# Kernel tuning notes

Measured on AMD Instinct MI355X. Metric: run time of the kernel, lower is better.

The kernel has to match this reference:

```python
import jax, jax.numpy as jnp
import numpy as np

N_NODES = 100000
N_EDGES = 1600000
EMBED = 64
HEADS = 8
HEAD_DIM = EMBED // HEADS
FFN = 4 * EMBED
EPS = 1e-5


def _layer_norm(x, g, b):
    m = jnp.mean(x, axis=-1, keepdims=True)
    v = jnp.mean(jnp.square(x - m), axis=-1, keepdims=True)
    return (x - m) * jax.lax.rsqrt(v + EPS) * g + b


def setup_inputs() -> dict:
    key = jax.random.key(0)
    ks = jax.random.split(key, 10)
    s = lambda fan_in: 1.0 / np.sqrt(fan_in)
    x = jax.random.normal(ks[0], (N_NODES, EMBED), dtype=jnp.float32)
    edge_indices = jax.random.randint(ks[1], (2, N_EDGES), 0, N_NODES, dtype=jnp.int64)
    attn_w = jax.random.uniform(ks[2], (EMBED, 3 * EMBED), jnp.float32, -s(EMBED), s(EMBED))
    attn_b = jnp.zeros((3 * EMBED,), jnp.float32)
    w1 = jax.random.uniform(ks[3], (EMBED, FFN), jnp.float32, -s(EMBED), s(EMBED))
    b1 = jnp.zeros((FFN,), jnp.float32)
    w2 = jax.random.uniform(ks[4], (FFN, EMBED), jnp.float32, -s(FFN), s(FFN))
    b2 = jnp.zeros((EMBED,), jnp.float32)
    ln1_g = jnp.ones((EMBED,), jnp.float32)
    ln1_b = jnp.zeros((EMBED,), jnp.float32)
    ln2_g = jnp.ones((EMBED,), jnp.float32)
    ln2_b = jnp.zeros((EMBED,), jnp.float32)
    return {"x": x, "edge_indices": edge_indices, "attn_w": attn_w, "attn_b": attn_b,
            "w1": w1, "b1": b1, "w2": w2, "b2": b2,
            "ln1_g": ln1_g, "ln1_b": ln1_b, "ln2_g": ln2_g, "ln2_b": ln2_b}


def _self_attention(x, edge_indices, attn_w, attn_b):
    n = x.shape[0]
    row, col = edge_indices[0], edge_indices[1]
    scale = EMBED ** (-0.5)  # note: original scales by embed_dim**-0.5
    qkv = (x @ attn_w + attn_b).reshape(n, HEADS, 3 * HEAD_DIM)
    q, k, v = jnp.split(qkv, 3, axis=2)  # each [N, H, Dh]
    alpha = jnp.sum(q[row] * k[col], axis=2) * scale  # [E, H]
    # sparse per-row softmax via segment reductions
    m = jax.ops.segment_max(alpha, row, num_segments=n)  # [N, H]
    e = jnp.exp(alpha - m[row])
    denom = jax.ops.segment_sum(e, row, num_segments=n)  # [N, H]
    weights = e / denom[row]  # [E, H]
    vals = v[col] * weights[:, :, None]  # [E, H, Dh]
    out = jax.ops.segment_sum(vals, row, num_segments=n)  # [N, H, Dh]
    return out.reshape(n, EMBED)


def reference(x, edge_indices, attn_w, attn_b, w1, b1, w2, b2, ln1_g, ln1_b, ln2_g, ln2_b):
    # post-norm (norm_first=False), dropout=0
    x = _layer_norm(x + _self_attention(x, edge_indices, attn_w, attn_b), ln1_g, ln1_b)
    ffn = jax.nn.relu(x @ w1 + b1) @ w2 + b2
    x = _layer_norm(x + ffn, ln2_g, ln2_b)
    return x
```

## Files before the change

kernel.cpp:

```cpp
#include <hip/hip_runtime.h>
#include <hip/hip_bf16.h>


#define WAVE 64
constexpr int BUCKET_SHIFT = 7;
constexpr int NBMAX = 800;

typedef __attribute__((ext_vector_type(8))) short bf16x8;
typedef __attribute__((ext_vector_type(4))) float f32x4;
typedef __attribute__((ext_vector_type(2))) float f32x2;
typedef __attribute__((ext_vector_type(2))) _Float16 h16x2;

__device__ __forceinline__ float bfbits_lo(unsigned u) {
  return __uint_as_float(u << 16);
}
__device__ __forceinline__ float bfbits_hi(unsigned u) {
  return __uint_as_float(u & 0xffff0000u);
}
__device__ __forceinline__ unsigned f2bf_pk(float a, float b) {
  unsigned ua = __float_as_uint(a);
  unsigned ub = __float_as_uint(b);
  ua = (ua + 0x7fff + ((ua >> 16) & 1)) >> 16;
  ub = (ub + 0x7fff + ((ub >> 16) & 1)) & 0xffff0000u;
  return ua | ub;
}
__device__ __forceinline__ unsigned short f2bf1(float a) {
  unsigned ua = __float_as_uint(a);
  ua = (ua + 0x7fff + ((ua >> 16) & 1)) >> 16;
  return (unsigned short)ua;
}

#if defined(__has_builtin)
#if __has_builtin(__builtin_amdgcn_cvt_pkrtz)
#define HAS_PKRTZ 1
#endif
#if __has_builtin(__builtin_amdgcn_fdot2)
#define HAS_FDOT2 1
#endif
#endif
#define EXP2F(x) exp2f(x)

__device__ __forceinline__ unsigned f2h_pk(float a, float b) {
#ifdef HAS_PKRTZ
  auto h = __builtin_amdgcn_cvt_pkrtz(a, b);
  return __builtin_bit_cast(unsigned, h);
#else
  h16x2 h;
  h.x = (_Float16)a;
  h.y = (_Float16)b;
  return __builtin_bit_cast(unsigned, h);
#endif
}

__device__ __forceinline__ float dot8_f16(uint4 kw, uint4 qw) {
#ifdef HAS_FDOT2
  float s = __builtin_amdgcn_fdot2(__builtin_bit_cast(h16x2, kw.x),
                                   __builtin_bit_cast(h16x2, qw.x), 0.f, false);
  s = __builtin_amdgcn_fdot2(__builtin_bit_cast(h16x2, kw.y),
                             __builtin_bit_cast(h16x2, qw.y), s, false);
  s = __builtin_amdgcn_fdot2(__builtin_bit_cast(h16x2, kw.z),
                             __builtin_bit_cast(h16x2, qw.z), s, false);
  s = __builtin_amdgcn_fdot2(__builtin_bit_cast(h16x2, kw.w),
                             __builtin_bit_cast(h16x2, qw.w), s, false);
  return s;
#else
  unsigned kk[4] = {kw.x, kw.y, kw.z, kw.w};
  unsigned qq[4] = {qw.x, qw.y, qw.z, qw.w};
  float s = 0.f;
#pragma unroll
  for (int i = 0; i < 4; i++) {
    h16x2 a = __builtin_bit_cast(h16x2, kk[i]);
    h16x2 b = __builtin_bit_cast(h16x2, qq[i]);
    s += (float)a.x * (float)b.x + (float)a.y * (float)b.y;
  }
  return s;
#endif
}

__device__ __forceinline__ void accmix8(uint4 w, float e, float acc[8]) {
  h16x2 p;
  p = __builtin_bit_cast(h16x2, w.x);
  acc[0] += (float)p.x * e;
  acc[1] += (float)p.y * e;
  p = __builtin_bit_cast(h16x2, w.y);
  acc[2] += (float)p.x * e;
  acc[3] += (float)p.y * e;
  p = __builtin_bit_cast(h16x2, w.z);
  acc[4] += (float)p.x * e;
  acc[5] += (float)p.y * e;
  p = __builtin_bit_cast(h16x2, w.w);
  acc[6] += (float)p.x * e;
  acc[7] += (float)p.y * e;
}

__global__ __launch_bounds__(256) void cvt_w2(
    const float* __restrict__ aw, const float* __restrict__ w1,
    const float* __restrict__ w2, unsigned short* __restrict__ awT,
    unsigned short* __restrict__ w1T, unsigned short* __restrict__ w2T) {
  int tid = blockIdx.x * 256 + threadIdx.x;
  int stride = gridDim.x * 256;
  for (int i = tid; i < 192 * 64; i += stride) {
    int nn = i >> 6, kk = i & 63;
    awT[i] = f2bf1(aw[kk * 192 + nn]);
  }
  for (int i = tid; i < 256 * 64; i += stride) {
    int nn = i >> 6, kk = i & 63;
    w1T[i] = f2bf1(w1[kk * 256 + nn]);
  }
  for (int i = tid; i < 64 * 256; i += stride) {
    int nn = i >> 8, kk = i & 255;
    w2T[i] = f2bf1(w2[kk * 64 + nn]);
  }
}

template <int NCOLS, int K, int MODE>
__global__ __launch_bounds__(256) void mfma_gemm(
    const unsigned short* __restrict__ A, const float* __restrict__ Af,
    const unsigned short* __restrict__ BT, const float* __restrict__ bias,
    unsigned short* __restrict__ out_q, unsigned char* __restrict__ out_kv,
    unsigned short* __restrict__ out_h,
    const unsigned short* __restrict__ resid, const float* __restrict__ g,
    const float* __restrict__ beta, float* __restrict__ out_f, int n) {
  constexpr int KP = K + 8;
  constexpr int NT = NCOLS / 16;
  constexpr int NKC = K / 32;
  __shared__ unsigned short sB[NCOLS * KP];

  const int tid = threadIdx.x;
  {
    const uint4* src = (const uint4*)BT;
    for (int idx = tid; idx < NCOLS * K / 8; idx += 256) {
      int nn = idx / (K / 8), kq = idx % (K / 8);
      *(uint4*)&sB[nn * KP + kq * 8] = src[idx];
    }
  }
  __syncthreads();

  const int wid = tid >> 6, lane = tid & 63;
  const int l15 = lane & 15, quad = lane >> 4;
  const int rowbase = blockIdx.x * 128 + wid * 32;

  bf16x8 afrag[2][NKC];
#pragma unroll
  for (int rg = 0; rg < 2; rg++) {
    int row = rowbase + rg * 16 + l15;
    if (row >= n) row = n - 1;
    if constexpr (MODE == 0) {
      const float4* ap = (const float4*)(Af + (size_t)row * K);
#pragma unroll
      for (int kc = 0; kc < NKC; kc++) {
        float4 a = ap[kc * 8 + quad * 2], b = ap[kc * 8 + quad * 2 + 1];
        union {
          unsigned u[4];
          bf16x8 v;
        } z;
        z.u[0] = f2bf_pk(a.x, a.y);
        z.u[1] = f2bf_pk(a.z, a.w);
        z.u[2] = f2bf_pk(b.x, b.y);
        z.u[3] = f2bf_pk(b.z, b.w);
        afrag[rg][kc] = z.v;
      }
    } else {
      const bf16x8* ap = (const bf16x8*)(A + (size_t)row * K);
#pragma unroll
      for (int kc = 0; kc < NKC; kc++) afrag[rg][kc] = ap[kc * 4 + quad];
    }
  }

  f32x4 acc[2][NT];
#pragma unroll
  for (int rg = 0; rg < 2; rg++)
#pragma unroll
    for (int t = 0; t < NT; t++) acc[rg][t] = (f32x4){0.f, 0.f, 0.f, 0.f};

#pragma unroll
  for (int t = 0; t < NT; t++) {
#pragma unroll
    for (int kc = 0; kc < NKC; kc++) {
      bf16x8 b = *(const bf16x8*)&sB[(t * 16 + l15) * KP + kc * 32 + quad * 8];
      acc[0][t] = __builtin_amdgcn_mfma_f32_16x16x32_bf16(b, afrag[0][kc],
                                                          acc[0][t], 0, 0, 0);
      acc[1][t] = __builtin_amdgcn_mfma_f32_16x16x32_bf16(b, afrag[1][kc],
                                                          acc[1][t], 0, 0, 0);
    }
  }

  if (MODE == 0) {
    constexpr float QSCALE = 0.125f * 1.44269504088896f;
#pragma unroll
    for (int rg = 0; rg < 2; rg++) {
      int row = rowbase + rg * 16 + l15;
      if (row >= n) continue;
#pragma unroll
      for (int t = 0; t < NT; t++) {
        int c0 = t * 16 + quad * 4;
        float4 bb = *(const float4*)&bias[c0];
        float v0 = acc[rg][t].x + bb.x, v1 = acc[rg][t].y + bb.y;
        float v2 = acc[rg][t].z + bb.z, v3 = acc[rg][t].w + bb.w;
        int hh = c0 / 24, rem = c0 % 24;
        if (rem < 8) {
          v0 *= QSCALE;
          v1 *= QSCALE;
          v2 *= QSCALE;
          v3 *= QSCALE;
          *(uint2*)(out_q + (size_t)row * 64 + hh * 8 + rem) =
              make_uint2(f2h_pk(v0, v1), f2h_pk(v2, v3));
        } else if (rem < 16) {
          *(uint2*)(out_kv + ((size_t)row << 8) + hh * 16 + (rem - 8) * 2) =
              make_uint2(f2h_pk(v0, v1), f2h_pk(v2, v3));
        } else {
          *(uint2*)(out_kv + ((size_t)row << 8) + 128 + hh * 16 +
                    (rem - 16) * 2) =
              make_uint2(f2h_pk(v0, v1), f2h_pk(v2, v3));
        }
      }
    }
  } else if (MODE == 1) {
#pragma unroll
    for (int rg = 0; rg < 2; rg++) {
      int row = rowbase + rg * 16 + l15;
      if (row >= n) continue;
#pragma unroll
      for (int t = 0; t < NT; t++) {
        int c0 = t * 16 + quad * 4;
        float4 bb = *(const float4*)&bias[c0];
        float v0 = fmaxf(acc[rg][t].x + bb.x, 0.f);
        float v1 = fmaxf(acc[rg][t].y + bb.y, 0.f);
        float v2 = fmaxf(acc[rg][t].z + bb.z, 0.f);
        float v3 = fmaxf(acc[rg][t].w + bb.w, 0.f);
        *(uint2*)(out_h + (size_t)row * NCOLS + c0) =
            make_uint2(f2bf_pk(v0, v1), f2bf_pk(v2, v3));
      }
    }
  } else {
#pragma unroll
    for (int rg = 0; rg < 2; rg++) {
      int row = rowbase + rg * 16 + l15;
      bool ok = row < n;
      int rowc = ok ? row : n - 1;
      float vals[4][4];
      float ps = 0.f, pq = 0.f;
#pragma unroll
      for (int t = 0; t < 4; t++) {
        int c0 = t * 16 + quad * 4;
        float4 bb = *(const float4*)&bias[c0];
        uint2 rr = *(const uint2*)&resid[(size_t)rowc * 64 + c0];
        vals[t][0] = acc[rg][t].x + bb.x + bfbits_lo(rr.x);
        vals[t][1] = acc[rg][t].y + bb.y + bfbits_hi(rr.x);
        vals[t][2] = acc[rg][t].z + bb.z + bfbits_lo(rr.y);
        vals[t][3] = acc[rg][t].w + bb.w + bfbits_hi(rr.y);
#pragma unroll
        for (int r = 0; r < 4; r++) {
          ps += vals[t][r];
          pq += vals[t][r] * vals[t][r];
        }
      }
      ps += __shfl_xor(ps, 16);
      ps += __shfl_xor(ps, 32);
      pq += __shfl_xor(pq, 16);
      pq += __shfl_xor(pq, 32);
      float mean = ps * (1.f / 64.f);
      float var = pq * (1.f / 64.f) - mean * mean;
      float inv = rsqrtf(var + 1e-5f);
      if (ok) {
#pragma unroll
        for (int t = 0; t < 4; t++) {
          int c0 = t * 16 + quad * 4;
          float4 gg = *(const float4*)&g[c0];
          float4 be = *(const float4*)&beta[c0];
          float4 o = make_float4((vals[t][0] - mean) * inv * gg.x + be.x,
                                 (vals[t][1] - mean) * inv * gg.y + be.y,
                                 (vals[t][2] - mean) * inv * gg.z + be.z,
                                 (vals[t][3] - mean) * inv * gg.w + be.w);
          *(float4*)&out_f[(size_t)row * 64 + c0] = o;
        }
      }
    }
  }
}

__device__ __forceinline__ int edge_row(const int* e, int i, bool is64) {
  return is64 ? e[2 * (size_t)i] : e[i];
}
__device__ __forceinline__ int edge_col(const int* e, int i, int E, bool is64) {
  return is64 ? e[2 * ((size_t)E + i)] : e[(size_t)E + i];
}

__global__ __launch_bounds__(256) void partition_count(
    const int* __restrict__ e, int E, int* __restrict__ G, int NB, int CH) {
  __shared__ int h[NBMAX];
  __shared__ int s32;
  if (threadIdx.x == 0) s32 = 0;
  for (int b = threadIdx.x; b < NB; b += 256) h[b] = 0;
  __syncthreads();
  unsigned v = 0;
  for (int i = threadIdx.x; i < 2048; i += 256) v |= (unsigned)e[2 * i + 1];
  if (v) s32 = 1;
  __syncthreads();
  bool is64 = (s32 == 0);
  int c0 = blockIdx.x * CH, c1 = min(E, c0 + CH);
  for (int i = c0 + threadIdx.x; i < c1; i += 256)
    atomicAdd(&h[edge_row(e, i, is64) >> BUCKET_SHIFT], 1);
  __syncthreads();
  for (int b = threadIdx.x; b < NB; b += 256) G[b * 256 + blockIdx.x] = h[b];
}

__global__ __launch_bounds__(1024) void scan_reduce(const int* __restrict__ in,
                                                    int n,
                                                    int* __restrict__ bsum) {
  __shared__ int sdata[16];
  int tid = threadIdx.x;
  int idx = blockIdx.x * 1024 + tid;
  int v = (idx < n) ? in[idx] : 0;
#pragma unroll
  for (int m = 1; m < WAVE; m <<= 1) v += __shfl_xor(v, m);
  if ((tid & 63) == 0) sdata[tid >> 6] = v;
  __syncthreads();
  if (tid < 16) {
    int s = sdata[tid];
#pragma unroll
    for (int m = 1; m < 16; m <<= 1) s += __shfl_xor(s, m);
    if (tid == 0) bsum[blockIdx.x] = s;
  }
}

__global__ __launch_bounds__(256) void scan_top(const int* __restrict__ bsum,
                                                int nb,
                                                int* __restrict__ bpre) {
  __shared__ int wsum[4];
  int tid = threadIdx.x;
  int lane = tid & 63, wid = tid >> 6;
  int v = (tid < nb) ? bsum[tid] : 0;
  int incl = v;
#pragma unroll
  for (int m = 1; m < WAVE; m <<= 1) {
    int t = __shfl_up(incl, m);
    if (lane >= m) incl += t;
  }
  if (lane == 63) wsum[wid] = incl;
  __syncthreads();
  int add = 0;
  for (int w = 0; w < wid; w++) add += wsum[w];
  if (tid < nb) bpre[tid] = add + incl - v;
}

__global__ __launch_bounds__(1024) void scan_apply(
    const int* __restrict__ in, int n, const int* __restrict__ bpre,
    int* __restrict__ outscan) {
  __shared__ int wtot[16];
  __shared__ int wexcl[16];
  int tid = threadIdx.x;
  int idx = blockIdx.x * 1024 + tid;
  int v = (idx < n) ? in[idx] : 0;
  int incl = v;
#pragma unroll
  for (int m = 1; m < WAVE; m <<= 1) {
    int t = __shfl_up(incl, m);
    if ((tid & 63) >= m) incl += t;
  }
  int wid = tid >> 6;
  if ((tid & 63) == 63) wtot[wid] = incl;
  __syncthreads();
  if (tid < 16) {
    int w = wtot[tid];
    int wi = w;
#pragma unroll
    for (int m = 1; m < 16; m <<= 1) {
      int t = __shfl_up(wi, m);
      if (tid >= m) wi += t;
    }
    wexcl[tid] = wi - w;
  }
  __syncthreads();
  if (idx < n) outscan[idx] = bpre[blockIdx.x] + wexcl[wid] + incl - v;
}

__global__ __launch_bounds__(256) void partition_scatter(
    const int* __restrict__ e, int E, const int* __restrict__ scanG,
    unsigned* __restrict__ ebuf, int NB, int CH) {
  __shared__ int base[NBMAX];
  __shared__ int s32;
  if (threadIdx.x == 0) s32 = 0;
  for (int b = threadIdx.x; b < NB; b += 256)
    base[b] = scanG[b * 256 + blockIdx.x];
  __syncthreads();
  unsigned v = 0;
  for (int i = threadIdx.x; i < 2048; i += 256) v |= (unsigned)e[2 * i + 1];
  if (v) s32 = 1;
  __syncthreads();
  bool is64 = (s32 == 0);
  int c0 = blockIdx.x * CH, c1 = min(E, c0 + CH);
  for (int i = c0 + threadIdx.x; i < c1; i += 256) {
    int r = edge_row(e, i, is64);
    int c = edge_col(e, i, E, is64);
    int pos = atomicAdd(&base[r >> BUCKET_SHIFT], 1);
    ebuf[pos] = ((unsigned)(r & 127) << 17) | (unsigned)c;
  }
}

__global__ __launch_bounds__(256) void bucket_csr(
    const unsigned* __restrict__ ebuf, const int* __restrict__ scanG,
    int* __restrict__ ecol, int* __restrict__ rowstart, int n, int NB, int E) {
  __shared__ int cnt[128], offs[128], cur[128];
  const int b = blockIdx.x;
  const int tid = threadIdx.x;
  const int start = scanG[b * 256];
  const int end = (b + 1 < NB) ? scanG[(b + 1) * 256] : E;
  if (tid < 128) cnt[tid] = 0;
  __syncthreads();
  for (int i = start + tid; i < end; i += 256)
    atomicAdd(&cnt[(ebuf[i] >> 17) & 127], 1);
  __syncthreads();
  if (tid < 128) offs[tid] = cnt[tid];
  __syncthreads();
  for (int s = 1; s < 128; s <<= 1) {
    int t = 0;
    if (tid < 128 && tid >= s) t = offs[tid - s];
    __syncthreads();
    if (tid < 128) offs[tid] += t;
    __syncthreads();
  }
  if (tid < 128) {
    int excl = offs[tid] - cnt[tid];
    cur[tid] = start + excl;
    int gr = (b << BUCKET_SHIFT) + tid;
    if (gr < n) rowstart[gr] = start + excl;
  }
  if (b == NB - 1 && tid == 0) rowstart[n] = E;
  __syncthreads();
  for (int i = start + tid; i < end; i += 256) {
    unsigned p = ebuf[i];
    int pos = atomicAdd(&cur[(p >> 17) & 127], 1);
    ecol[pos] = (int)(p & 0x1FFFF);
  }
}

__global__ __launch_bounds__(256) void attn_ln_kernel(
    const float* __restrict__ x, const unsigned short* __restrict__ qbuf,
    const unsigned char* __restrict__ kv, const int* __restrict__ rowstart,
    const int* __restrict__ ecol, const float* __restrict__ g,
    const float* __restrict__ beta, unsigned short* __restrict__ x1b, int n) {
  int wave = threadIdx.x >> 6;
  int lane = threadIdx.x & 63;
  int node0 = (blockIdx.x * 4 + wave) * 2;
  if (node0 >= n) return;
  const int e = lane >> 4;
  const int h = lane & 7;
  int node = node0 + ((lane >> 3) & 1);
  bool nvalid = node < n;
  int nodec = nvalid ? node : n - 1;

  uint4 qp = ((const uint4*)qbuf)[(size_t)nodec * 8 + h];

  const float* xr = x + (size_t)nodec * 64 + h * 8;
  float4 x0 = *(const float4*)xr;
  float4 x1 = *(const float4*)(xr + 4);

  int start = rowstart[nodec];
  int cnt = nvalid ? rowstart[nodec + 1] - start : 0;
  const int* ec = ecol + start;
  const int koff = h * 16, voff = 128 + h * 16;

  float den = 0.f;
  float acc[8] = {0.f, 0.f, 0.f, 0.f, 0.f, 0.f, 0.f, 0.f};

  int iters = (cnt + 3) >> 2;
  int maxit = max(iters, __shfl_xor(iters, 8));

  int it = 0;
  for (; it + 2 <= maxit; it += 2) {
    int i0 = it * 4 + e;
    int i1 = i0 + 4;
    bool b0 = i0 < cnt;
    bool b1 = i1 < cnt;
    int c0 = ec[b0 ? i0 : 0] & 0x1FFFF;
    int c1 = ec[b1 ? i1 : 0] & 0x1FFFF;
    const unsigned char* r0 = kv + ((size_t)c0 << 8);
    const unsigned char* r1 = kv + ((size_t)c1 << 8);
    uint4 kw0 = *(const uint4*)(r0 + koff);
    uint4 vw0 = *(const uint4*)(r0 + voff);
    uint4 kw1 = *(const uint4*)(r1 + koff);
    uint4 vw1 = *(const uint4*)(r1 + voff);
    float a0 = dot8_f16(kw0, qp);
    float a1 = dot8_f16(kw1, qp);
    float e0 = b0 ? EXP2F(a0) : 0.f;
    float e1 = b1 ? EXP2F(a1) : 0.f;
    den += e0 + e1;
    accmix8(vw0, e0, acc);
    accmix8(vw1, e1, acc);
  }
  if (it < maxit) {
    int i0 = it * 4 + e;
    bool b0 = i0 < cnt;
    int c0 = ec[b0 ? i0 : 0] & 0x1FFFF;
    const unsigned char* r0 = kv + ((size_t)c0 << 8);
    uint4 kw0 = *(const uint4*)(r0 + koff);
    uint4 vw0 = *(const uint4*)(r0 + voff);
    float a0 = dot8_f16(kw0, qp);
    float e0 = b0 ? EXP2F(a0) : 0.f;
    den += e0;
    accmix8(vw0, e0, acc);
  }

#pragma unroll
  for (int m = 16; m < 64; m <<= 1) {
    den += __shfl_xor(den, m);
#pragma unroll
    for (int j = 0; j < 8; j++) acc[j] += __shfl_xor(acc[j], m);
  }

  float invden = (cnt > 0) ? 1.f / den : 0.f;

  float v[8];
  v[0] = x0.x + acc[0] * invden;
  v[1] = x0.y + acc[1] * invden;
  v[2] = x0.z + acc[2] * invden;
  v[3] = x0.w + acc[3] * invden;
  v[4] = x1.x + acc[4] * invden;
  v[5] = x1.y + acc[5] * invden;
  v[6] = x1.z + acc[6] * invden;
  v[7] = x1.w + acc[7] * invden;

  float ps = 0.f;
#pragma unroll
  for (int j = 0; j < 8; j++) ps += v[j];
#pragma unroll
  for (int m = 1; m < 8; m <<= 1) ps += __shfl_xor(ps, m);
  float mean = ps * (1.f / 64.f);
  float pq = 0.f;
#pragma unroll
  for (int j = 0; j < 8; j++) {
    float d = v[j] - mean;
    pq += d * d;
  }
#pragma unroll
  for (int m = 1; m < 8; m <<= 1) pq += __shfl_xor(pq, m);
  float inv = rsqrtf(pq * (1.f / 64.f) + 1e-5f);

  if (e == 0 && nvalid) {
    const float4* gr = (const float4*)(g + h * 8);
    const float4* br = (const float4*)(beta + h * 8);
    float4 ga = gr[0], gb = gr[1];
    float4 ba = br[0], bb = br[1];
    float o[8];
    o[0] = (v[0] - mean) * inv * ga.x + ba.x;
    o[1] = (v[1] - mean) * inv * ga.y + ba.y;
    o[2] = (v[2] - mean) * inv * ga.z + ba.z;
    o[3] = (v[3] - mean) * inv * ga.w + ba.w;
    o[4] = (v[4] - mean) * inv * gb.x + bb.x;
    o[5] = (v[5] - mean) * inv * gb.y + bb.y;
    o[6] = (v[6] - mean) * inv * gb.z + bb.z;
    o[7] = (v[7] - mean) * inv * gb.w + bb.w;
    *(uint4*)(x1b + (size_t)node * 64 + h * 8) =
        make_uint4(f2bf_pk(o[0], o[1]), f2bf_pk(o[2], o[3]),
                   f2bf_pk(o[4], o[5]), f2bf_pk(o[6], o[7]));
  }
}

extern "C" void kernel_launch(void* const* d_in, const int* in_sizes, int n_in,
                              void* d_out, int out_size, void* d_ws,
                              size_t ws_size, hipStream_t stream) {
  const float* x = (const float*)d_in[0];
  const int* edges = (const int*)d_in[1];
  const float* attn_w = (const float*)d_in[2];
  const float* attn_b = (const float*)d_in[3];
  const float* w1 = (const float*)d_in[4];
  const float* b1 = (const float*)d_in[5];
  const float* w2 = (const float*)d_in[6];
  const float* b2 = (const float*)d_in[7];
  const float* g1 = (const float*)d_in[8];
  const float* bb1 = (const float*)d_in[9];
  const float* g2 = (const float*)d_in[10];
  const float* bb2 = (const float*)d_in[11];

  const int N = in_sizes[0] / 64;
  const int E = in_sizes[1] / 2;
  const int NB = (N + 127) >> BUCKET_SHIFT;
  const int CH = (E + 255) / 256;
  const int NG = NB * 256;

  char* ws = (char*)d_ws;
  size_t oq = 0;
  size_t okv = oq + (size_t)N * 128;
  size_t ox1b = okv + (size_t)N * 256;
  size_t oh = ox1b + (size_t)N * 128;
  size_t oawT = oh + (size_t)N * 512;
  size_t ow1T = oawT + 192 * 64 * 2;
  size_t ow2T = ow1T + 256 * 64 * 2;
  size_t oG = ow2T + 64 * 256 * 2;
  size_t oscanG = oG + (size_t)NG * 4;
  size_t oebuf = oscanG + (size_t)NG * 4;
  size_t oecol = oebuf + (size_t)E * 4;
  size_t orowstart = oecol + (size_t)E * 4;
  size_t obsum = orowstart + (size_t)(N + 4) * 4;
  size_t obpre = obsum + 1024;

  unsigned short* qbuf = (unsigned short*)(ws + oq);
  unsigned char* kvb = (unsigned char*)(ws + okv);
  unsigned short* x1b = (unsigned short*)(ws + ox1b);
  unsigned short* hbuf = (unsigned short*)(ws + oh);
  unsigned short* awT = (unsigned short*)(ws + oawT);
  unsigned short* w1T = (unsigned short*)(ws + ow1T);
  unsigned short* w2T = (unsigned short*)(ws + ow2T);
  int* G = (int*)(ws + oG);
  int* scanG = (int*)(ws + oscanG);
  unsigned* ebuf = (unsigned*)(ws + oebuf);
  int* ecol = (int*)(ws + oecol);
  int* rowstart = (int*)(ws + orowstart);
  int* bsum = (int*)(ws + obsum);
  int* bpre = (int*)(ws + obpre);

  cvt_w2<<<32, 256, 0, stream>>>(attn_w, w1, w2, awT, w1T, w2T);

  partition_count<<<256, 256, 0, stream>>>(edges, E, G, NB, CH);
  int nscan = (NG + 1023) / 1024;
  scan_reduce<<<nscan, 1024, 0, stream>>>(G, NG, bsum);
  scan_top<<<1, 256, 0, stream>>>(bsum, nscan, bpre);
  scan_apply<<<nscan, 1024, 0, stream>>>(G, NG, bpre, scanG);
  partition_scatter<<<256, 256, 0, stream>>>(edges, E, scanG, ebuf, NB, CH);
  bucket_csr<<<NB, 256, 0, stream>>>(ebuf, scanG, ecol, rowstart, N, NB, E);

  const int gblocks = (N + 127) / 128;

  mfma_gemm<192, 64, 0><<<gblocks, 256, 0, stream>>>(
      nullptr, x, awT, attn_b, qbuf, kvb, nullptr, nullptr, nullptr, nullptr,
      nullptr, N);

  attn_ln_kernel<<<(N + 7) / 8, 256, 0, stream>>>(x, qbuf, kvb, rowstart, ecol,
                                                  g1, bb1, x1b, N);

  mfma_gemm<256, 64, 1><<<gblocks, 256, 0, stream>>>(
      x1b, nullptr, w1T, b1, nullptr, nullptr, hbuf, nullptr, nullptr, nullptr,
      nullptr, N);

  mfma_gemm<64, 256, 2><<<gblocks, 256, 0, stream>>>(
      hbuf, nullptr, w2T, b2, nullptr, nullptr, nullptr, x1b, g2, bb2,
      (float*)d_out, N);
}
```

Measured before the change: 289.9 us.

## Increase edge-partition block count and halve GEMM rows per block

Raises the partition_count/partition_scatter grid from 256 to 1024 blocks, with a smaller edge chunk per block. The histogram matrix and the scan grow to match, and scan_top becomes a 1024-thread looping scan that can handle more than 256 partial sums. The MFMA GEMMs now give each wave 16 rows instead of 32, doubling the number of blocks so more of the GPU is busy. The int64 edge reads use an int2 view. In exchange, the scan has four times more histogram entries to process, and each GEMM block loads the shared B tile while reusing it across fewer rows.

```diff
diff --git a/kernel.cpp b/kernel.cpp
--- a/kernel.cpp
+++ b/kernel.cpp
@@ -5,6 +5,7 @@
 #define WAVE 64
 constexpr int BUCKET_SHIFT = 7;
 constexpr int NBMAX = 800;
+constexpr int NBLK = 1024;
 
 typedef __attribute__((ext_vector_type(8))) short bf16x8;
 typedef __attribute__((ext_vector_type(4))) float f32x4;
@@ -138,65 +139,54 @@
 
   const int wid = tid >> 6, lane = tid & 63;
   const int l15 = lane & 15, quad = lane >> 4;
-  const int rowbase = blockIdx.x * 128 + wid * 32;
-
-  bf16x8 afrag[2][NKC];
-#pragma unroll
-  for (int rg = 0; rg < 2; rg++) {
-    int row = rowbase + rg * 16 + l15;
-    if (row >= n) row = n - 1;
-    if constexpr (MODE == 0) {
-      const float4* ap = (const float4*)(Af + (size_t)row * K);
-#pragma unroll
-      for (int kc = 0; kc < NKC; kc++) {
-        float4 a = ap[kc * 8 + quad * 2], b = ap[kc * 8 + quad * 2 + 1];
-        union {
-          unsigned u[4];
-          bf16x8 v;
-        } z;
-        z.u[0] = f2bf_pk(a.x, a.y);
-        z.u[1] = f2bf_pk(a.z, a.w);
-        z.u[2] = f2bf_pk(b.x, b.y);
-        z.u[3] = f2bf_pk(b.z, b.w);
-        afrag[rg][kc] = z.v;
-      }
-    } else {
-      const bf16x8* ap = (const bf16x8*)(A + (size_t)row * K);
-#pragma unroll
-      for (int kc = 0; kc < NKC; kc++) afrag[rg][kc] = ap[kc * 4 + quad];
-    }
-  }
-
-  f32x4 acc[2][NT];
-#pragma unroll
-  for (int rg = 0; rg < 2; rg++)
-#pragma unroll
-    for (int t = 0; t < NT; t++) acc[rg][t] = (f32x4){0.f, 0.f, 0.f, 0.f};
+  const int row0 = blockIdx.x * 64 + wid * 16 + l15;
+  const int row = (row0 < n) ? row0 : (n - 1);
+
+  bf16x8 afrag[NKC];
+  if constexpr (MODE == 0) {
+    const float4* ap = (const float4*)(Af + (size_t)row * K);
+#pragma unroll
+    for (int kc = 0; kc < NKC; kc++) {
+      float4 a = ap[kc * 8 + quad * 2], b = ap[kc * 8 + quad * 2 + 1];
+      union {
+        unsigned u[4];
+        bf16x8 v;
+      } z;
+      z.u[0] = f2bf_pk(a.x, a.y);
+      z.u[1] = f2bf_pk(a.z, a.w);
+      z.u[2] = f2bf_pk(b.x, b.y);
+      z.u[3] = f2bf_pk(b.z, b.w);
+      afrag[kc] = z.v;
+    }
+  } else {
+    const bf16x8* ap = (const bf16x8*)(A + (size_t)row * K);
+#pragma unroll
+    for (int kc = 0; kc < NKC; kc++) afrag[kc] = ap[kc * 4 + quad];
+  }
+
+  f32x4 acc[NT];
+#pragma unroll
+  for (int t = 0; t < NT; t++) acc[t] = (f32x4){0.f, 0.f, 0.f, 0.f};
 
 #pragma unroll
   for (int t = 0; t < NT; t++) {
 #pragma unroll
     for (int kc = 0; kc < NKC; kc++) {
       bf16x8 b = *(const bf16x8*)&sB[(t * 16 + l15) * KP + kc * 32 + quad * 8];
-      acc[0][t] = __builtin_amdgcn_mfma_f32_16x16x32_bf16(b, afrag[0][kc],
-                                                          acc[0][t], 0, 0, 0);
-      acc[1][t] = __builtin_amdgcn_mfma_f32_16x16x32_bf16(b, afrag[1][kc],
-                                                          acc[1][t], 0, 0, 0);
+      acc[t] =
+          __builtin_amdgcn_mfma_f32_16x16x32_bf16(b, afrag[kc], acc[t], 0, 0, 0);
     }
   }
 
   if (MODE == 0) {
     constexpr float QSCALE = 0.125f * 1.44269504088896f;
-#pragma unroll
-    for (int rg = 0; rg < 2; rg++) {
-      int row = rowbase + rg * 16 + l15;
-      if (row >= n) continue;
+    if (row0 < n) {
 #pragma unroll
       for (int t = 0; t < NT; t++) {
         int c0 = t * 16 + quad * 4;
         float4 bb = *(const float4*)&bias[c0];
-        float v0 = acc[rg][t].x + bb.x, v1 = acc[rg][t].y + bb.y;
-        float v2 = acc[rg][t].z + bb.z, v3 = acc[rg][t].w + bb.w;
+        float v0 = acc[t].x + bb.x, v1 = acc[t].y + bb.y;
+        float v2 = acc[t].z + bb.z, v3 = acc[t].w + bb.w;
         int hh = c0 / 24, rem = c0 % 24;
         if (rem < 8) {
           v0 *= QSCALE;
@@ -216,74 +206,66 @@
       }
     }
   } else if (MODE == 1) {
-#pragma unroll
-    for (int rg = 0; rg < 2; rg++) {
-      int row = rowbase + rg * 16 + l15;
-      if (row >= n) continue;
+    if (row0 < n) {
 #pragma unroll
       for (int t = 0; t < NT; t++) {
         int c0 = t * 16 + quad * 4;
         float4 bb = *(const float4*)&bias[c0];
-        float v0 = fmaxf(acc[rg][t].x + bb.x, 0.f);
-        float v1 = fmaxf(acc[rg][t].y + bb.y, 0.f);
-        float v2 = fmaxf(acc[rg][t].z + bb.z, 0.f);
-        float v3 = fmaxf(acc[rg][t].w + bb.w, 0.f);
+        float v0 = fmaxf(acc[t].x + bb.x, 0.f);
+        float v1 = fmaxf(acc[t].y + bb.y, 0.f);
+        float v2 = fmaxf(acc[t].z + bb.z, 0.f);
+        float v3 = fmaxf(acc[t].w + bb.w, 0.f);
         *(uint2*)(out_h + (size_t)row * NCOLS + c0) =
             make_uint2(f2bf_pk(v0, v1), f2bf_pk(v2, v3));
       }
     }
   } else {
-#pragma unroll
-    for (int rg = 0; rg < 2; rg++) {
-      int row = rowbase + rg * 16 + l15;
-      bool ok = row < n;
-      int rowc = ok ? row : n - 1;
-      float vals[4][4];
-      float ps = 0.f, pq = 0.f;
+    bool ok = row0 < n;
+    float vals[4][4];
+    float ps = 0.f, pq = 0.f;
+#pragma unroll
+    for (int t = 0; t < 4; t++) {
+      int c0 = t * 16 + quad * 4;
+      float4 bb = *(const float4*)&bias[c0];
+      uint2 rr = *(const uint2*)&resid[(size_t)row * 64 + c0];
+      vals[t][0] = acc[t].x + bb.x + bfbits_lo(rr.x);
+      vals[t][1] = acc[t].y + bb.y + bfbits_hi(rr.x);
+      vals[t][2] = acc[t].z + bb.z + bfbits_lo(rr.y);
+      vals[t][3] = acc[t].w + bb.w + bfbits_hi(rr.y);
+#pragma unroll
+      for (int r = 0; r < 4; r++) {
+        ps += vals[t][r];
+        pq += vals[t][r] * vals[t][r];
+      }
+    }
+    ps += __shfl_xor(ps, 16);
+    ps += __shfl_xor(ps, 32);
+    pq += __shfl_xor(pq, 16);
+    pq += __shfl_xor(pq, 32);
+    float mean = ps * (1.f / 64.f);
+    float var = pq * (1.f / 64.f) - mean * mean;
+    float inv = rsqrtf(var + 1e-5f);
+    if (ok) {
 #pragma unroll
       for (int t = 0; t < 4; t++) {
         int c0 = t * 16 + quad * 4;
-        float4 bb = *(const float4*)&bias[c0];
-        uint2 rr = *(const uint2*)&resid[(size_t)rowc * 64 + c0];
-        vals[t][0] = acc[rg][t].x + bb.x + bfbits_lo(rr.x);
-        vals[t][1] = acc[rg][t].y + bb.y + bfbits_hi(rr.x);
-        vals[t][2] = acc[rg][t].z + bb.z + bfbits_lo(rr.y);
-        vals[t][3] = acc[rg][t].w + bb.w + bfbits_hi(rr.y);
-#pragma unroll
-        for (int r = 0; r < 4; r++) {
-          ps += vals[t][r];
-          pq += vals[t][r] * vals[t][r];
-        }
+        float4 gg = *(const float4*)&g[c0];
+        float4 be = *(const float4*)&beta[c0];
+        float4 o = make_float4((vals[t][0] - mean) * inv * gg.x + be.x,
+                               (vals[t][1] - mean) * inv * gg.y + be.y,
+                               (vals[t][2] - mean) * inv * gg.z + be.z,
+                               (vals[t][3] - mean) * inv * gg.w + be.w);
+        *(float4*)&out_f[(size_t)row * 64 + c0] = o;
       }
-      ps += __shfl_xor(ps, 16);
-      ps += __shfl_xor(ps, 32);
-      pq += __shfl_xor(pq, 16);
-      pq += __shfl_xor(pq, 32);
-      float mean = ps * (1.f / 64.f);
-      float var = pq * (1.f / 64.f) - mean * mean;
-      float inv = rsqrtf(var + 1e-5f);
-      if (ok) {
-#pragma unroll
-        for (int t = 0; t < 4; t++) {
-          int c0 = t * 16 + quad * 4;
-          float4 gg = *(const float4*)&g[c0];
-          float4 be = *(const float4*)&beta[c0];
-          float4 o = make_float4((vals[t][0] - mean) * inv * gg.x + be.x,
-                                 (vals[t][1] - mean) * inv * gg.y + be.y,
-                                 (vals[t][2] - mean) * inv * gg.z + be.z,
-                                 (vals[t][3] - mean) * inv * gg.w + be.w);
-          *(float4*)&out_f[(size_t)row * 64 + c0] = o;
-        }
-      }
     }
   }
 }
 
 __device__ __forceinline__ int edge_row(const int* e, int i, bool is64) {
-  return is64 ? e[2 * (size_t)i] : e[i];
+  return is64 ? ((const int2*)e)[i].x : e[i];
 }
 __device__ __forceinline__ int edge_col(const int* e, int i, int E, bool is64) {
-  return is64 ? e[2 * ((size_t)E + i)] : e[(size_t)E + i];
+  return is64 ? ((const int2*)e)[(size_t)E + i].x : e[(size_t)E + i];
 }
 
 __global__ __launch_bounds__(256) void partition_count(
@@ -302,7 +284,7 @@
   for (int i = c0 + threadIdx.x; i < c1; i += 256)
     atomicAdd(&h[edge_row(e, i, is64) >> BUCKET_SHIFT], 1);
   __syncthreads();
-  for (int b = threadIdx.x; b < NB; b += 256) G[b * 256 + blockIdx.x] = h[b];
+  for (int b = threadIdx.x; b < NB; b += 256) G[b * NBLK + blockIdx.x] = h[b];
 }
 
 __global__ __launch_bounds__(1024) void scan_reduce(const int* __restrict__ in,
@@ -324,24 +306,36 @@
   }
 }
 
-__global__ __launch_bounds__(256) void scan_top(const int* __restrict__ bsum,
-                                                int nb,
-                                                int* __restrict__ bpre) {
-  __shared__ int wsum[4];
-  int tid = threadIdx.x;
-  int lane = tid & 63, wid = tid >> 6;
-  int v = (tid < nb) ? bsum[tid] : 0;
-  int incl = v;
-#pragma unroll
-  for (int m = 1; m < WAVE; m <<= 1) {
-    int t = __shfl_up(incl, m);
-    if (lane >= m) incl += t;
-  }
-  if (lane == 63) wsum[wid] = incl;
-  __syncthreads();
-  int add = 0;
-  for (int w = 0; w < wid; w++) add += wsum[w];
-  if (tid < nb) bpre[tid] = add + incl - v;
+__global__ __launch_bounds__(1024) void scan_top(const int* __restrict__ bsum,
+                                                 int nb,
+                                                 int* __restrict__ bpre) {
+  __shared__ int wsum[16];
+  __shared__ int carry;
+  int tid = threadIdx.x, lane = tid & 63, wid = tid >> 6;
+  if (tid == 0) carry = 0;
+  __syncthreads();
+  for (int base = 0; base < nb; base += 1024) {
+    int idx = base + tid;
+    int v = (idx < nb) ? bsum[idx] : 0;
+    int incl = v;
+#pragma unroll
+    for (int m = 1; m < WAVE; m <<= 1) {
+      int t = __shfl_up(incl, m);
+      if (lane >= m) incl += t;
+    }
+    if (lane == 63) wsum[wid] = incl;
+    __syncthreads();
+    int add = carry;
+    for (int w = 0; w < wid; w++) add += wsum[w];
+    if (idx < nb) bpre[idx] = add + incl - v;
+    __syncthreads();
+    if (tid == 0) {
+      int t = 0;
+      for (int w = 0; w < 16; w++) t += wsum[w];
+      carry += t;
+    }
+    __syncthreads();
+  }
 }
 
 __global__ __launch_bounds__(1024) void scan_apply(
@@ -382,7 +376,7 @@
   __shared__ int s32;
   if (threadIdx.x == 0) s32 = 0;
   for (int b = threadIdx.x; b < NB; b += 256)
-    base[b] = scanG[b * 256 + blockIdx.x];
+    base[b] = scanG[b * NBLK + blockIdx.x];
   __syncthreads();
   unsigned v = 0;
   for (int i = threadIdx.x; i < 2048; i += 256) v |= (unsigned)e[2 * i + 1];
@@ -404,8 +398,8 @@
   __shared__ int cnt[128], offs[128], cur[128];
   const int b = blockIdx.x;
   const int tid = threadIdx.x;
-  const int start = scanG[b * 256];
-  const int end = (b + 1 < NB) ? scanG[(b + 1) * 256] : E;
+  const int start = scanG[b * NBLK];
+  const int end = (b + 1 < NB) ? scanG[(b + 1) * NBLK] : E;
   if (tid < 128) cnt[tid] = 0;
   __syncthreads();
   for (int i = start + tid; i < end; i += 256)
@@ -576,8 +570,8 @@
   const int N = in_sizes[0] / 64;
   const int E = in_sizes[1] / 2;
   const int NB = (N + 127) >> BUCKET_SHIFT;
-  const int CH = (E + 255) / 256;
-  const int NG = NB * 256;
+  const int CH = (E + NBLK - 1) / NBLK;
+  const int NG = NB * NBLK;
 
   char* ws = (char*)d_ws;
   size_t oq = 0;
@@ -593,7 +587,7 @@
   size_t oecol = oebuf + (size_t)E * 4;
   size_t orowstart = oecol + (size_t)E * 4;
   size_t obsum = orowstart + (size_t)(N + 4) * 4;
-  size_t obpre = obsum + 1024;
+  size_t obpre = obsum + 4096;
 
   unsigned short* qbuf = (unsigned short*)(ws + oq);
   unsigned char* kvb = (unsigned char*)(ws + okv);
@@ -612,15 +606,15 @@
 
   cvt_w2<<<32, 256, 0, stream>>>(attn_w, w1, w2, awT, w1T, w2T);
 
-  partition_count<<<256, 256, 0, stream>>>(edges, E, G, NB, CH);
+  partition_count<<<NBLK, 256, 0, stream>>>(edges, E, G, NB, CH);
   int nscan = (NG + 1023) / 1024;
   scan_reduce<<<nscan, 1024, 0, stream>>>(G, NG, bsum);
-  scan_top<<<1, 256, 0, stream>>>(bsum, nscan, bpre);
+  scan_top<<<1, 1024, 0, stream>>>(bsum, nscan, bpre);
   scan_apply<<<nscan, 1024, 0, stream>>>(G, NG, bpre, scanG);
-  partition_scatter<<<256, 256, 0, stream>>>(edges, E, scanG, ebuf, NB, CH);
+  partition_scatter<<<NBLK, 256, 0, stream>>>(edges, E, scanG, ebuf, NB, CH);
   bucket_csr<<<NB, 256, 0, stream>>>(ebuf, scanG, ecol, rowstart, N, NB, E);
 
-  const int gblocks = (N + 127) / 128;
+  const int gblocks = (N + 63) / 64;
 
   mfma_gemm<192, 64, 0><<<gblocks, 256, 0, stream>>>(
       nullptr, x, awT, attn_b, qbuf, kvb, nullptr, nullptr, nullptr, nullptr,
```

New measurement: 297.5 us. 2.6% more time.

## Collapse edge partition pipeline into fewer kernels and switch GEMMs to fp16

Applied to the files above, without the earlier changes.

Replaces the seven-kernel CSR build (count, three-pass scan, scatter, bucket) with a memset plus three kernels. Global bucket counts are now accumulated with atomics, and each block scans those counts locally, so the separate scan launches go away. The weight conversion is folded into the counting kernel. All bf16 intermediates and MFMAs are switched to fp16, which gives more mantissa bits but a narrower range. The scatter order now depends on atomics, so the edge order inside a bucket is no longer deterministic.

```diff
diff --git a/kernel.cpp b/kernel.cpp
--- a/kernel.cpp
+++ b/kernel.cpp
@@ -1,55 +1,28 @@
 #include <hip/hip_runtime.h>
-#include <hip/hip_bf16.h>
 
 
 #define WAVE 64
 constexpr int BUCKET_SHIFT = 7;
 constexpr int NBMAX = 800;
 
-typedef __attribute__((ext_vector_type(8))) short bf16x8;
+typedef __attribute__((ext_vector_type(8))) short s16x8;
 typedef __attribute__((ext_vector_type(4))) float f32x4;
-typedef __attribute__((ext_vector_type(2))) float f32x2;
 typedef __attribute__((ext_vector_type(2))) _Float16 h16x2;
-
-__device__ __forceinline__ float bfbits_lo(unsigned u) {
-  return __uint_as_float(u << 16);
-}
-__device__ __forceinline__ float bfbits_hi(unsigned u) {
-  return __uint_as_float(u & 0xffff0000u);
-}
-__device__ __forceinline__ unsigned f2bf_pk(float a, float b) {
-  unsigned ua = __float_as_uint(a);
-  unsigned ub = __float_as_uint(b);
-  ua = (ua + 0x7fff + ((ua >> 16) & 1)) >> 16;
-  ub = (ub + 0x7fff + ((ub >> 16) & 1)) & 0xffff0000u;
-  return ua | ub;
-}
-__device__ __forceinline__ unsigned short f2bf1(float a) {
-  unsigned ua = __float_as_uint(a);
-  ua = (ua + 0x7fff + ((ua >> 16) & 1)) >> 16;
-  return (unsigned short)ua;
-}
+typedef __attribute__((ext_vector_type(8))) __fp16 fp16x8;
 
 #if defined(__has_builtin)
-#if __has_builtin(__builtin_amdgcn_cvt_pkrtz)
-#define HAS_PKRTZ 1
-#endif
 #if __has_builtin(__builtin_amdgcn_fdot2)
 #define HAS_FDOT2 1
 #endif
 #endif
 #define EXP2F(x) exp2f(x)
 
+__device__ __forceinline__ unsigned short f2h1(float a) {
+  _Float16 h = (_Float16)a;
+  return __builtin_bit_cast(unsigned short, h);
+}
 __device__ __forceinline__ unsigned f2h_pk(float a, float b) {
-#ifdef HAS_PKRTZ
-  auto h = __builtin_amdgcn_cvt_pkrtz(a, b);
-  return __builtin_bit_cast(unsigned, h);
-#else
-  h16x2 h;
-  h.x = (_Float16)a;
-  h.y = (_Float16)b;
-  return __builtin_bit_cast(unsigned, h);
-#endif
+  return (unsigned)f2h1(a) | ((unsigned)f2h1(b) << 16);
 }
 
 __device__ __forceinline__ float dot8_f16(uint4 kw, uint4 qw) {
@@ -93,23 +66,152 @@
   acc[7] += (float)p.y * e;
 }
 
-__global__ __launch_bounds__(256) void cvt_w2(
+__device__ __forceinline__ int edge_row(const int* e, int i, bool is64) {
+  return is64 ? e[2 * (size_t)i] : e[i];
+}
+__device__ __forceinline__ int edge_col(const int* e, int i, int E, bool is64) {
+  return is64 ? e[2 * ((size_t)E + i)] : e[(size_t)E + i];
+}
+
+__device__ __forceinline__ void scan_buckets(const int* __restrict__ bcnt,
+                                             int NB, int* sb) {
+  __shared__ int ws_[4];
+  int tid = threadIdx.x;
+  int t0 = tid * 4;
+  int v0 = 0, v1 = 0, v2 = 0, v3 = 0;
+  if (t0 + 0 < NB) v0 = bcnt[t0 + 0];
+  if (t0 + 1 < NB) v1 = bcnt[t0 + 1];
+  if (t0 + 2 < NB) v2 = bcnt[t0 + 2];
+  if (t0 + 3 < NB) v3 = bcnt[t0 + 3];
+  int s = v0 + v1 + v2 + v3;
+  int lane = tid & 63, wid = tid >> 6;
+  int incl = s;
+#pragma unroll
+  for (int m = 1; m < WAVE; m <<= 1) {
+    int t = __shfl_up(incl, m);
+    if (lane >= m) incl += t;
+  }
+  if (lane == 63) ws_[wid] = incl;
+  __syncthreads();
+  int add = 0;
+  for (int w = 0; w < wid; w++) add += ws_[w];
+  int base = add + incl - s;
+  if (t0 + 0 < NB) sb[t0 + 0] = base;
+  base += v0;
+  if (t0 + 1 < NB) sb[t0 + 1] = base;
+  base += v1;
+  if (t0 + 2 < NB) sb[t0 + 2] = base;
+  base += v2;
+  if (t0 + 3 < NB) sb[t0 + 3] = base;
+  __syncthreads();
+}
+
+__global__ __launch_bounds__(256) void prep_kernel(
     const float* __restrict__ aw, const float* __restrict__ w1,
     const float* __restrict__ w2, unsigned short* __restrict__ awT,
-    unsigned short* __restrict__ w1T, unsigned short* __restrict__ w2T) {
-  int tid = blockIdx.x * 256 + threadIdx.x;
+    unsigned short* __restrict__ w1T, unsigned short* __restrict__ w2T,
+    const int* __restrict__ e, int E, int* __restrict__ bcnt, int NB, int CH) {
+  int gtid = blockIdx.x * 256 + threadIdx.x;
   int stride = gridDim.x * 256;
-  for (int i = tid; i < 192 * 64; i += stride) {
+  for (int i = gtid; i < 192 * 64; i += stride) {
     int nn = i >> 6, kk = i & 63;
-    awT[i] = f2bf1(aw[kk * 192 + nn]);
-  }
-  for (int i = tid; i < 256 * 64; i += stride) {
+    awT[i] = f2h1(aw[kk * 192 + nn]);
+  }
+  for (int i = gtid; i < 256 * 64; i += stride) {
     int nn = i >> 6, kk = i & 63;
-    w1T[i] = f2bf1(w1[kk * 256 + nn]);
-  }
-  for (int i = tid; i < 64 * 256; i += stride) {
+    w1T[i] = f2h1(w1[kk * 256 + nn]);
+  }
+  for (int i = gtid; i < 64 * 256; i += stride) {
     int nn = i >> 8, kk = i & 255;
-    w2T[i] = f2bf1(w2[kk * 64 + nn]);
+    w2T[i] = f2h1(w2[kk * 64 + nn]);
+  }
+  __shared__ int h[NBMAX];
+  __shared__ int s32;
+  if (threadIdx.x == 0) s32 = 0;
+  for (int b = threadIdx.x; b < NB; b += 256) h[b] = 0;
+  __syncthreads();
+  unsigned v = 0;
+  for (int i = threadIdx.x; i < 2048; i += 256) v |= (unsigned)e[2 * i + 1];
+  if (v) s32 = 1;
+  __syncthreads();
+  bool is64 = (s32 == 0);
+  int c0 = blockIdx.x * CH, c1 = min(E, c0 + CH);
+  for (int i = c0 + threadIdx.x; i < c1; i += 256)
+    atomicAdd(&h[edge_row(e, i, is64) >> BUCKET_SHIFT], 1);
+  __syncthreads();
+  for (int b = threadIdx.x; b < NB; b += 256)
+    if (h[b]) atomicAdd(&bcnt[b], h[b]);
+}
+
+__global__ __launch_bounds__(256) void scatter_kernel(
+    const int* __restrict__ e, int E, const int* __restrict__ bcnt,
+    int* __restrict__ gcur, unsigned* __restrict__ ebuf, int NB, int CH) {
+  __shared__ int h[NBMAX];
+  __shared__ int sb[NBMAX];
+  __shared__ int cur[NBMAX];
+  __shared__ int s32;
+  if (threadIdx.x == 0) s32 = 0;
+  for (int b = threadIdx.x; b < NB; b += 256) h[b] = 0;
+  __syncthreads();
+  unsigned v = 0;
+  for (int i = threadIdx.x; i < 2048; i += 256) v |= (unsigned)e[2 * i + 1];
+  if (v) s32 = 1;
+  __syncthreads();
+  bool is64 = (s32 == 0);
+  int c0 = blockIdx.x * CH, c1 = min(E, c0 + CH);
+  for (int i = c0 + threadIdx.x; i < c1; i += 256)
+    atomicAdd(&h[edge_row(e, i, is64) >> BUCKET_SHIFT], 1);
+  __syncthreads();
+  scan_buckets(bcnt, NB, sb);
+  for (int b = threadIdx.x; b < NB; b += 256) {
+    int hb = h[b];
+    cur[b] = hb ? (sb[b] + atomicAdd(&gcur[b], hb)) : 0;
+  }
+  __syncthreads();
+  for (int i = c0 + threadIdx.x; i < c1; i += 256) {
+    int r = edge_row(e, i, is64);
+    int c = edge_col(e, i, E, is64);
+    int pos = atomicAdd(&cur[r >> BUCKET_SHIFT], 1);
+    ebuf[pos] = ((unsigned)(r & 127) << 17) | (unsigned)c;
+  }
+}
+
+__global__ __launch_bounds__(256) void bucket_csr(
+    const unsigned* __restrict__ ebuf, const int* __restrict__ bcnt,
+    int* __restrict__ ecol, int* __restrict__ rowstart, int n, int NB, int E) {
+  __shared__ int cnt[128], offs[128], cur[128];
+  __shared__ int sb[NBMAX];
+  scan_buckets(bcnt, NB, sb);
+  const int b = blockIdx.x;
+  const int tid = threadIdx.x;
+  const int start = sb[b];
+  const int end = (b + 1 < NB) ? sb[b + 1] : E;
+  if (tid < 128) cnt[tid] = 0;
+  __syncthreads();
+  for (int i = start + tid; i < end; i += 256)
+    atomicAdd(&cnt[(ebuf[i] >> 17) & 127], 1);
+  __syncthreads();
+  if (tid < 128) offs[tid] = cnt[tid];
+  __syncthreads();
+  for (int s = 1; s < 128; s <<= 1) {
+    int t = 0;
+    if (tid < 128 && tid >= s) t = offs[tid - s];
+    __syncthreads();
+    if (tid < 128) offs[tid] += t;
+    __syncthreads();
+  }
+  if (tid < 128) {
+    int excl = offs[tid] - cnt[tid];
+    cur[tid] = start + excl;
+    int gr = (b << BUCKET_SHIFT) + tid;
+    if (gr < n) rowstart[gr] = start + excl;
+  }
+  if (b == NB - 1 && tid == 0) rowstart[n] = E;
+  __syncthreads();
+  for (int i = start + tid; i < end; i += 256) {
+    unsigned p = ebuf[i];
+    int pos = atomicAdd(&cur[(p >> 17) & 127], 1);
+    ecol[pos] = (int)(p & 0x1FFFF);
   }
 }
 
@@ -140,7 +242,7 @@
   const int l15 = lane & 15, quad = lane >> 4;
   const int rowbase = blockIdx.x * 128 + wid * 32;
 
-  bf16x8 afrag[2][NKC];
+  s16x8 afrag[2][NKC];
 #pragma unroll
   for (int rg = 0; rg < 2; rg++) {
     int row = rowbase + rg * 16 + l15;
@@ -152,16 +254,16 @@
         float4 a = ap[kc * 8 + quad * 2], b = ap[kc * 8 + quad * 2 + 1];
         union {
           unsigned u[4];
-          bf16x8 v;
+          s16x8 v;
         } z;
-        z.u[0] = f2bf_pk(a.x, a.y);
-        z.u[1] = f2bf_pk(a.z, a.w);
-        z.u[2] = f2bf_pk(b.x, b.y);
-        z.u[3] = f2bf_pk(b.z, b.w);
+        z.u[0] = f2h_pk(a.x, a.y);
+        z.u[1] = f2h_pk(a.z, a.w);
+        z.u[2] = f2h_pk(b.x, b.y);
+        z.u[3] = f2h_pk(b.z, b.w);
         afrag[rg][kc] = z.v;
       }
     } else {
-      const bf16x8* ap = (const bf16x8*)(A + (size_t)row * K);
+      const s16x8* ap = (const s16x8*)(A + (size_t)row * K);
 #pragma unroll
       for (int kc = 0; kc < NKC; kc++) afrag[rg][kc] = ap[kc * 4 + quad];
     }
@@ -177,11 +279,12 @@
   for (int t = 0; t < NT; t++) {
 #pragma unroll
     for (int kc = 0; kc < NKC; kc++) {
-      bf16x8 b = *(const bf16x8*)&sB[(t * 16 + l15) * KP + kc * 32 + quad * 8];
-      acc[0][t] = __builtin_amdgcn_mfma_f32_16x16x32_bf16(b, afrag[0][kc],
-                                                          acc[0][t], 0, 0, 0);
-      acc[1][t] = __builtin_amdgcn_mfma_f32_16x16x32_bf16(b, afrag[1][kc],
-                                                          acc[1][t], 0, 0, 0);
+      s16x8 b = *(const s16x8*)&sB[(t * 16 + l15) * KP + kc * 32 + quad * 8];
+      fp16x8 bh = __builtin_bit_cast(fp16x8, b);
+      acc[0][t] = __builtin_amdgcn_mfma_f32_16x16x32_f16(
+          bh, __builtin_bit_cast(fp16x8, afrag[0][kc]), acc[0][t], 0, 0, 0);
+      acc[1][t] = __builtin_amdgcn_mfma_f32_16x16x32_f16(
+          bh, __builtin_bit_cast(fp16x8, afrag[1][kc]), acc[1][t], 0, 0, 0);
     }
   }
 
@@ -229,7 +332,7 @@
         float v2 = fmaxf(acc[rg][t].z + bb.z, 0.f);
         float v3 = fmaxf(acc[rg][t].w + bb.w, 0.f);
         *(uint2*)(out_h + (size_t)row * NCOLS + c0) =
-            make_uint2(f2bf_pk(v0, v1), f2bf_pk(v2, v3));
+            make_uint2(f2h_pk(v0, v1), f2h_pk(v2, v3));
       }
     }
   } else {
@@ -245,10 +348,12 @@
         int c0 = t * 16 + quad * 4;
         float4 bb = *(const float4*)&bias[c0];
         uint2 rr = *(const uint2*)&resid[(size_t)rowc * 64 + c0];
-        vals[t][0] = acc[rg][t].x + bb.x + bfbits_lo(rr.x);
-        vals[t][1] = acc[rg][t].y + bb.y + bfbits_hi(rr.x);
-        vals[t][2] = acc[rg][t].z + bb.z + bfbits_lo(rr.y);
-        vals[t][3] = acc[rg][t].w + bb.w + bfbits_hi(rr.y);
+        h16x2 ra = __builtin_bit_cast(h16x2, rr.x);
+        h16x2 rb = __builtin_bit_cast(h16x2, rr.y);
+        vals[t][0] = acc[rg][t].x + bb.x + (float)ra.x;
+        vals[t][1] = acc[rg][t].y + bb.y + (float)ra.y;
+        vals[t][2] = acc[rg][t].z + bb.z + (float)rb.x;
+        vals[t][3] = acc[rg][t].w + bb.w + (float)rb.y;
 #pragma unroll
         for (int r = 0; r < 4; r++) {
           ps += vals[t][r];
@@ -276,162 +381,6 @@
         }
       }
     }
-  }
-}
-
-__device__ __forceinline__ int edge_row(const int* e, int i, bool is64) {
-  return is64 ? e[2 * (size_t)i] : e[i];
-}
-__device__ __forceinline__ int edge_col(const int* e, int i, int E, bool is64) {
-  return is64 ? e[2 * ((size_t)E + i)] : e[(size_t)E + i];
-}
-
-__global__ __launch_bounds__(256) void partition_count(
-    const int* __restrict__ e, int E, int* __restrict__ G, int NB, int CH) {
-  __shared__ int h[NBMAX];
-  __shared__ int s32;
-  if (threadIdx.x == 0) s32 = 0;
-  for (int b = threadIdx.x; b < NB; b += 256) h[b] = 0;
-  __syncthreads();
-  unsigned v = 0;
-  for (int i = threadIdx.x; i < 2048; i += 256) v |= (unsigned)e[2 * i + 1];
-  if (v) s32 = 1;
-  __syncthreads();
-  bool is64 = (s32 == 0);
-  int c0 = blockIdx.x * CH, c1 = min(E, c0 + CH);
-  for (int i = c0 + threadIdx.x; i < c1; i += 256)
-    atomicAdd(&h[edge_row(e, i, is64) >> BUCKET_SHIFT], 1);
-  __syncthreads();
-  for (int b = threadIdx.x; b < NB; b += 256) G[b * 256 + blockIdx.x] = h[b];
-}
-
-__global__ __launch_bounds__(1024) void scan_reduce(const int* __restrict__ in,
-                                                    int n,
-                                                    int* __restrict__ bsum) {
-  __shared__ int sdata[16];
-  int tid = threadIdx.x;
-  int idx = blockIdx.x * 1024 + tid;
-  int v = (idx < n) ? in[idx] : 0;
-#pragma unroll
-  for (int m = 1; m < WAVE; m <<= 1) v += __shfl_xor(v, m);
-  if ((tid & 63) == 0) sdata[tid >> 6] = v;
-  __syncthreads();
-  if (tid < 16) {
-    int s = sdata[tid];
-#pragma unroll
-    for (int m = 1; m < 16; m <<= 1) s += __shfl_xor(s, m);
-    if (tid == 0) bsum[blockIdx.x] = s;
-  }
-}
-
-__global__ __launch_bounds__(256) void scan_top(const int* __restrict__ bsum,
-                                                int nb,
-                                                int* __restrict__ bpre) {
-  __shared__ int wsum[4];
-  int tid = threadIdx.x;
-  int lane = tid & 63, wid = tid >> 6;
-  int v = (tid < nb) ? bsum[tid] : 0;
-  int incl = v;
-#pragma unroll
-  for (int m = 1; m < WAVE; m <<= 1) {
-    int t = __shfl_up(incl, m);
-    if (lane >= m) incl += t;
-  }
-  if (lane == 63) wsum[wid] = incl;
-  __syncthreads();
-  int add = 0;
-  for (int w = 0; w < wid; w++) add += wsum[w];
-  if (tid < nb) bpre[tid] = add + incl - v;
-}
-
-__global__ __launch_bounds__(1024) void scan_apply(
-    const int* __restrict__ in, int n, const int* __restrict__ bpre,
-    int* __restrict__ outscan) {
-  __shared__ int wtot[16];
-  __shared__ int wexcl[16];
-  int tid = threadIdx.x;
-  int idx = blockIdx.x * 1024 + tid;
-  int v = (idx < n) ? in[idx] : 0;
-  int incl = v;
-#pragma unroll
-  for (int m = 1; m < WAVE; m <<= 1) {
-    int t = __shfl_up(incl, m);
-    if ((tid & 63) >= m) incl += t;
-  }
-  int wid = tid >> 6;
-  if ((tid & 63) == 63) wtot[wid] = incl;
-  __syncthreads();
-  if (tid < 16) {
-    int w = wtot[tid];
-    int wi = w;
-#pragma unroll
-    for (int m = 1; m < 16; m <<= 1) {
-      int t = __shfl_up(wi, m);
-      if (tid >= m) wi += t;
-    }
-    wexcl[tid] = wi - w;
-  }
-  __syncthreads();
-  if (idx < n) outscan[idx] = bpre[blockIdx.x] + wexcl[wid] + incl - v;
-}
-
-__global__ __launch_bounds__(256) void partition_scatter(
-    const int* __restrict__ e, int E, const int* __restrict__ scanG,
-    unsigned* __restrict__ ebuf, int NB, int CH) {
-  __shared__ int base[NBMAX];
-  __shared__ int s32;
-  if (threadIdx.x == 0) s32 = 0;
-  for (int b = threadIdx.x; b < NB; b += 256)
-    base[b] = scanG[b * 256 + blockIdx.x];
-  __syncthreads();
-  unsigned v = 0;
-  for (int i = threadIdx.x; i < 2048; i += 256) v |= (unsigned)e[2 * i + 1];
-  if (v) s32 = 1;
-  __syncthreads();
-  bool is64 = (s32 == 0);
-  int c0 = blockIdx.x * CH, c1 = min(E, c0 + CH);
-  for (int i = c0 + threadIdx.x; i < c1; i += 256) {
-    int r = edge_row(e, i, is64);
-    int c = edge_col(e, i, E, is64);
-    int pos = atomicAdd(&base[r >> BUCKET_SHIFT], 1);
-    ebuf[pos] = ((unsigned)(r & 127) << 17) | (unsigned)c;
-  }
-}
-
-__global__ __launch_bounds__(256) void bucket_csr(
-    const unsigned* __restrict__ ebuf, const int* __restrict__ scanG,
-    int* __restrict__ ecol, int* __restrict__ rowstart, int n, int NB, int E) {
-  __shared__ int cnt[128], offs[128], cur[128];
-  const int b = blockIdx.x;
-  const int tid = threadIdx.x;
-  const int start = scanG[b * 256];
-  const int end = (b + 1 < NB) ? scanG[(b + 1) * 256] : E;
-  if (tid < 128) cnt[tid] = 0;
-  __syncthreads();
-  for (int i = start + tid; i < end; i += 256)
-    atomicAdd(&cnt[(ebuf[i] >> 17) & 127], 1);
-  __syncthreads();
-  if (tid < 128) offs[tid] = cnt[tid];
-  __syncthreads();
-  for (int s = 1; s < 128; s <<= 1) {
-    int t = 0;
-    if (tid < 128 && tid >= s) t = offs[tid - s];
-    __syncthreads();
-    if (tid < 128) offs[tid] += t;
-    __syncthreads();
-  }
-  if (tid < 128) {
-    int excl = offs[tid] - cnt[tid];
-    cur[tid] = start + excl;
-    int gr = (b << BUCKET_SHIFT) + tid;
-    if (gr < n) rowstart[gr] = start + excl;
-  }
-  if (b == NB - 1 && tid == 0) rowstart[n] = E;
-  __syncthreads();
-  for (int i = start + tid; i < end; i += 256) {
-    unsigned p = ebuf[i];
-    int pos = atomicAdd(&cur[(p >> 17) & 127], 1);
-    ecol[pos] = (int)(p & 0x1FFFF);
   }
 }
 
@@ -552,8 +501,8 @@
     o[6] = (v[6] - mean) * inv * gb.z + bb.z;
     o[7] = (v[7] - mean) * inv * gb.w + bb.w;
     *(uint4*)(x1b + (size_t)node * 64 + h * 8) =
-        make_uint4(f2bf_pk(o[0], o[1]), f2bf_pk(o[2], o[3]),
-                   f2bf_pk(o[4], o[5]), f2bf_pk(o[6], o[7]));
+        make_uint4(f2h_pk(o[0], o[1]), f2h_pk(o[2], o[3]),
+                   f2h_pk(o[4], o[5]), f2h_pk(o[6], o[7]));
   }
 }
 
@@ -577,7 +526,6 @@
   const int E = in_sizes[1] / 2;
   const int NB = (N + 127) >> BUCKET_SHIFT;
   const int CH = (E + 255) / 256;
-  const int NG = NB * 256;
 
   char* ws = (char*)d_ws;
   size_t oq = 0;
@@ -587,13 +535,11 @@
   size_t oawT = oh + (size_t)N * 512;
   size_t ow1T = oawT + 192 * 64 * 2;
   size_t ow2T = ow1T + 256 * 64 * 2;
-  size_t oG = ow2T + 64 * 256 * 2;
-  size_t oscanG = oG + (size_t)NG * 4;
-  size_t oebuf = oscanG + (size_t)NG * 4;
+  size_t obcnt = ow2T + 64 * 256 * 2;
+  size_t ogcur = obcnt + NBMAX * 4;
+  size_t oebuf = ogcur + NBMAX * 4;
   size_t oecol = oebuf + (size_t)E * 4;
   size_t orowstart = oecol + (size_t)E * 4;
-  size_t obsum = orowstart + (size_t)(N + 4) * 4;
-  size_t obpre = obsum + 1024;
 
   unsigned short* qbuf = (unsigned short*)(ws + oq);
   unsigned char* kvb = (unsigned char*)(ws + okv);
@@ -602,23 +548,18 @@
   unsigned short* awT = (unsigned short*)(ws + oawT);
   unsigned short* w1T = (unsigned short*)(ws + ow1T);
   unsigned short* w2T = (unsigned short*)(ws + ow2T);
-  int* G = (int*)(ws + oG);
-  int* scanG = (int*)(ws + oscanG);
+  int* bcnt = (int*)(ws + obcnt);
+  int* gcur = (int*)(ws + ogcur);
   unsigned* ebuf = (unsigned*)(ws + oebuf);
   int* ecol = (int*)(ws + oecol);
   int* rowstart = (int*)(ws + orowstart);
-  int* bsum = (int*)(ws + obsum);
-  int* bpre = (int*)(ws + obpre);
-
-  cvt_w2<<<32, 256, 0, stream>>>(attn_w, w1, w2, awT, w1T, w2T);
-
-  partition_count<<<256, 256, 0, stream>>>(edges, E, G, NB, CH);
-  int nscan = (NG + 1023) / 1024;
-  scan_reduce<<<nscan, 1024, 0, stream>>>(G, NG, bsum);
-  scan_top<<<1, 256, 0, stream>>>(bsum, nscan, bpre);
-  scan_apply<<<nscan, 1024, 0, stream>>>(G, NG, bpre, scanG);
-  partition_scatter<<<256, 256, 0, stream>>>(edges, E, scanG, ebuf, NB, CH);
-  bucket_csr<<<NB, 256, 0, stream>>>(ebuf, scanG, ecol, rowstart, N, NB, E);
+
+  (void)hipMemsetAsync(bcnt, 0, NBMAX * 8, stream);
+
+  prep_kernel<<<256, 256, 0, stream>>>(attn_w, w1, w2, awT, w1T, w2T, edges, E,
+                                       bcnt, NB, CH);
+  scatter_kernel<<<256, 256, 0, stream>>>(edges, E, bcnt, gcur, ebuf, NB, CH);
+  bucket_csr<<<NB, 256, 0, stream>>>(ebuf, bcnt, ecol, rowstart, N, NB, E);
 
   const int gblocks = (N + 127) / 128;
 
```

Measured after the change: 286.8 us. Within noise of the previous version (-1.1%).
